# Kernel tuning notes

Measured on AMD Instinct MI355X. Metric: run time of the kernel, lower is better.

## Reference

```python
import math
import jax, jax.numpy as jnp
from jax import lax
import numpy as np

THETA = 10.0      # spiking threshold
TAU_SR = 10.0     # SRM (psp) alpha-kernel time constant
TAU_REF = 1.0     # refractory alpha-kernel time constant
SCALE_REF = 2.0   # refractory scale (kernel = -scaleRef*theta*alpha)
TAU_RHO = 1.0     # surrogate-gradient width
TS = 1.0          # simulation time step


def _alpha_filter_scan(x, tau, extra_input_fn=None):
    """Causal convolution along last (time) axis with alpha kernel
    k[n] = (n*Ts/tau) * exp(1 - n*Ts/tau)  (k[0] = 0),
    implemented exactly as a 2-state linear recurrence.
    x: [N, C, T] -> out: [N, C, T]."""
    d = jnp.float32(math.exp(-TS / tau))
    c = jnp.float32(math.e * TS / tau)
    xT = jnp.moveaxis(x, -1, 0)  # [T, N, C]

    def step(carry, xt):
        p, a = carry
        a = d * (a + p)          # alpha response from inputs up to t-1
        p = d * p + xt           # pure exponential state
        return (p, a), a * c

    z = jnp.zeros_like(xT[0])
    _, out = lax.scan(step, (z, z), xT)
    return jnp.moveaxis(out, 0, -1)


def psp(x):
    return _alpha_filter_scan(x, TAU_SR)


@jax.custom_vjp
def spike_fn(v):
    # Heaviside threshold on (membrane - theta)
    return (v >= 0).astype(v.dtype)

def _spike_fwd(v):
    return spike_fn(v), v

def _spike_bwd(v, g):
    # SLAYER surrogate gradient: exponential pdf around threshold
    grad = (1.0 / TAU_RHO) * jnp.exp(-jnp.abs(v) / TAU_RHO)
    return (g * grad,)

spike_fn.defvjp(_spike_fwd, _spike_bwd)


def spike_layer(u_in):
    """Threshold-and-refract over time. u_in: [N, C, T] psp potentials.
    Refractory response = -scaleRef*theta * alpha_{tauRef}(past spikes)."""
    d = jnp.float32(math.exp(-TS / TAU_REF))
    c = jnp.float32(math.e * TS / TAU_REF)
    ref_scale = jnp.float32(-SCALE_REF * THETA)
    uT = jnp.moveaxis(u_in, -1, 0)  # [T, N, C]

    def step(carry, ut):
        p, a = carry
        a = d * (a + p)                      # refractory potential at t
        u = ut + c * a                       # membrane potential
        s = spike_fn(u - THETA)              # spikes (0/1)
        p = d * p + ref_scale * s            # inject refractory impulse
        return (p, a), s

    z = jnp.zeros_like(uT[0])
    _, s = lax.scan(step, (z, z), uT)
    return jnp.moveaxis(s, 0, -1)


def setup_inputs() -> dict:
    key = jax.random.key(0)
    k1, k2, k3 = jax.random.split(key, 3)
    N, I, H, O, T = 64, 256, 1024, 18, 500
    # Bernoulli(0.1) input spikes
    spike_input = (jax.random.uniform(k1, (N, I, T)) < 0.1).astype(jnp.float32)
    W1 = jax.random.normal(k2, (H, I), dtype=jnp.float32) * (1.0 / math.sqrt(I))
    W2 = jax.random.normal(k3, (O, H), dtype=jnp.float32) * (1.0 / math.sqrt(H))
    return {"spike_input": spike_input, "W1": W1, "W2": W2}


def reference(spike_input, W1, W2):
    # layer 1: dense (per-timestep linear) -> psp -> spike
    y1 = jnp.einsum('nit,hi->nht', spike_input, W1)
    s1 = spike_layer(psp(y1))
    # layer 2
    y2 = jnp.einsum('nht,oh->not', s1, W2)
    s2 = spike_layer(psp(y2))
    return s2
```

## Files before the change

kernel.cpp:

```cpp
#include <hip/hip_runtime.h>


#define NN 64
#define II 256
#define HH 1024
#define OO 18
#define TT 500

#define D_SR 0.9048374180359595f
#define C_SR 0.27182818284590454f
#define D_RF 0.36787944117144233f
#define C_RF 2.718281828459045f
#define THETA 10.0f
#define REFS (-20.0f)

typedef _Float16 f16;
typedef _Float16 f16x2 __attribute__((ext_vector_type(2)));
typedef _Float16 f16x8 __attribute__((ext_vector_type(8)));
typedef float f32x4 __attribute__((ext_vector_type(4)));

__device__ __forceinline__ void gl2lds16(const void* g, void* l) {
    __builtin_amdgcn_global_load_lds(
        (const __attribute__((address_space(1))) void*)g,
        (__attribute__((address_space(3))) void*)l, 16, 0, 0);
}

__launch_bounds__(256)
__global__ void prep_x(const float* __restrict__ X, f16* __restrict__ Xb) {
    __shared__ float tile[64][65];
    const int n = blockIdx.z, i0 = blockIdx.y * 64, t0 = blockIdx.x * 64;
    const int tx = threadIdx.x & 63, q = threadIdx.x >> 6;
    const float* Xn = X + (size_t)n * II * TT;
#pragma unroll 4
    for (int j = 0; j < 16; ++j) {
        int il = j * 4 + q;
        int t = t0 + tx;
        tile[il][tx] = (t < TT) ? Xn[(size_t)(i0 + il) * TT + t] : 0.f;
    }
    __syncthreads();
#pragma unroll 4
    for (int j = 0; j < 16; ++j) {
        int tl = j * 4 + q;
        int t = t0 + tl;
        if (t < TT)
            Xb[((size_t)n * TT + t) * II + i0 + tx] = (f16)tile[tx][tl];
    }
}

__launch_bounds__(256)
__global__ void prep_w1(const float* __restrict__ W1, f16* __restrict__ Wh,
                        f16* __restrict__ Wl) {
    int idx = blockIdx.x * 256 + threadIdx.x;
    float w = W1[idx];
    f16 h = (f16)w;
    f16 l = (f16)(w - (float)h);
    Wh[idx] = h;
    Wl[idx] = l;
}

__launch_bounds__(256)
__global__ void prep_w2(const float* __restrict__ W2, f16* __restrict__ Wh,
                        f16* __restrict__ Wl) {
    int idx = blockIdx.x * 256 + threadIdx.x;
    int o = idx >> 10;
    float w = (o < OO) ? W2[idx] : 0.f;
    f16 h = (f16)w;
    f16 l = (f16)(w - (float)h);
    Wh[idx] = h;
    Wl[idx] = l;
}

__launch_bounds__(256)
__global__ void gemm1_scan1(const f16* __restrict__ Xb, const f16* __restrict__ Wh,
                            const f16* __restrict__ Wl, f16* __restrict__ S1) {
    __shared__ __align__(16) char smem[128 * 132 * 4];
    float* yb = (float*)smem;

    const int tid = threadIdx.x;
    const int wave = tid >> 6, lane = tid & 63;

    const int f = blockIdx.y * 8 + blockIdx.x;
    const int x = f & 7, g = f >> 3;
    const int n = x * 8 + (g & 7);
    const int ht = g >> 3;
    const int h0g = ht * 128;

    const int rbl = wave * 32 + (lane >> 2);
    const int koff = (lane & 3) * 8;
    const f16* gBh0 = Wh + (size_t)(h0g + rbl) * II + koff;
    const f16* gBl0 = Wl + (size_t)(h0g + rbl) * II + koff;

    const int wm = wave & 1, wn = wave >> 1;
    const int fr = lane & 15, kq = lane >> 4;

    float p1 = 0.f, a1 = 0.f, p2 = 0.f, a2 = 0.f;

    for (int c = 0; c < 4; ++c) {
        const int t0 = c * 128;
        const int TCe = (TT - t0 < 128) ? (TT - t0) : 128;

        int r0 = rbl;      if (r0 > TCe - 1) r0 = TCe - 1;
        int r1 = rbl + 16; if (r1 > TCe - 1) r1 = TCe - 1;
        const f16* gA0 = Xb + ((size_t)n * TT + t0 + r0) * II + koff;
        const f16* gA1 = Xb + ((size_t)n * TT + t0 + r1) * II + koff;

        auto stage = [&](int kk2, int b) {
            f16* As_b = (f16*)(smem + b * 24576);
            f16* Bh_b = As_b + 4096;
            f16* Bl_b = As_b + 8192;
            const int ko = kk2 * 32;
            gl2lds16(gA0 + ko, As_b + wave * 1024);
            gl2lds16(gA1 + ko, As_b + wave * 1024 + 512);
            gl2lds16(gBh0 + ko, Bh_b + wave * 1024);
            gl2lds16(gBh0 + 16 * II + ko, Bh_b + wave * 1024 + 512);
            gl2lds16(gBl0 + ko, Bl_b + wave * 1024);
            gl2lds16(gBl0 + 16 * II + ko, Bl_b + wave * 1024 + 512);
        };

        stage(0, 0);

        f32x4 acc[4][4] = {};
        for (int kk = 0; kk < 8; ++kk) {
            __syncthreads();
            if (kk < 7) stage(kk + 1, (kk + 1) & 1);

            const f16* As_b = (const f16*)(smem + (kk & 1) * 24576);
            const f16* Bh_b = As_b + 4096;
            const f16* Bl_b = As_b + 8192;

            f16x8 av[4], bhv[4], blv[4];
#pragma unroll
            for (int i = 0; i < 4; ++i) {
                av[i]  = *(const f16x8*)(As_b + (wm * 64 + i * 16 + fr) * 32 + kq * 8);
                bhv[i] = *(const f16x8*)(Bh_b + (wn * 64 + i * 16 + fr) * 32 + kq * 8);
                blv[i] = *(const f16x8*)(Bl_b + (wn * 64 + i * 16 + fr) * 32 + kq * 8);
            }
#pragma unroll
            for (int i = 0; i < 4; ++i)
#pragma unroll
                for (int j = 0; j < 4; ++j) {
                    acc[i][j] = __builtin_amdgcn_mfma_f32_16x16x32_f16(av[i], bhv[j], acc[i][j], 0, 0, 0);
                    acc[i][j] = __builtin_amdgcn_mfma_f32_16x16x32_f16(av[i], blv[j], acc[i][j], 0, 0, 0);
                }
        }
        __syncthreads();

#pragma unroll
        for (int i = 0; i < 4; ++i)
#pragma unroll
            for (int j = 0; j < 4; ++j) {
                int tr = wm * 64 + i * 16 + kq * 4;
                int hc = wn * 64 + j * 16 + fr;
#pragma unroll
                for (int r = 0; r < 4; ++r)
                    yb[(tr + r) * 132 + hc] = acc[i][j][r];
            }
        __syncthreads();

        if (tid < 128) {
            f16* sq = S1 + ((size_t)n * TT + t0) * HH + h0g + tid;
            float rb_[8];
#pragma unroll
            for (int j = 0; j < 8; ++j) rb_[j] = yb[j * 132 + tid];
            int t = 0;
            for (; t + 8 <= TCe; t += 8) {
#pragma unroll
                for (int j = 0; j < 8; ++j) {
                    float xv = rb_[j];
                    int tn = t + j + 8;
                    rb_[j] = (tn < TCe) ? yb[tn * 132 + tid] : 0.f;
                    a1 = D_SR * (a1 + p1);
                    p1 = D_SR * p1 + xv;
                    float ut = C_SR * a1;
                    a2 = D_RF * (a2 + p2);
                    float u = ut + C_RF * a2;
                    float s = (u >= THETA) ? 1.0f : 0.0f;
                    p2 = D_RF * p2 + REFS * s;
                    sq[(size_t)(t + j) * HH] = (f16)s;
                }
            }
            int rem = TCe - t;
#pragma unroll
            for (int j = 0; j < 8; ++j) {
                if (j < rem) {
                    float xv = rb_[j];
                    a1 = D_SR * (a1 + p1);
                    p1 = D_SR * p1 + xv;
                    float ut = C_SR * a1;
                    a2 = D_RF * (a2 + p2);
                    float u = ut + C_RF * a2;
                    float s = (u >= THETA) ? 1.0f : 0.0f;
                    p2 = D_RF * p2 + REFS * s;
                    sq[(size_t)(t + j) * HH] = (f16)s;
                }
            }
        }
        __syncthreads();
    }
}

__launch_bounds__(256)
__global__ void gemm2_mfma(const f16* __restrict__ S1, const f16* __restrict__ W2h,
                           const f16* __restrict__ W2l, float* __restrict__ Y2) {
    __shared__ __align__(16) f16 As[2][64 * 32];
    __shared__ __align__(16) f16 Bh[2][32 * 32];
    __shared__ __align__(16) f16 Bl[2][32 * 32];

    const int tid = threadIdx.x;
    const int wave = tid >> 6, lane = tid & 63;
    const int m0 = blockIdx.x * 64;
    const int fr = lane & 15, kq = lane >> 4;

    const f16* gA = S1 + (size_t)(m0 + wave * 16 + (lane >> 2)) * HH + (lane & 3) * 8;
    const f16* gB = (wave < 2 ? W2h : W2l) + (size_t)((wave & 1) * 16 + (lane >> 2)) * HH + (lane & 3) * 8;

    auto stage = [&](int kk2, int b) {
        const int ko = kk2 * 32;
        gl2lds16(gA + ko, &As[b][wave * 512]);
        gl2lds16(gB + ko, (wave < 2 ? &Bh[b][0] : &Bl[b][0]) + (wave & 1) * 512);
    };

    stage(0, 0);

    f32x4 acc[2] = {};
    for (int kk = 0; kk < HH / 32; ++kk) {
        __syncthreads();
        if (kk < HH / 32 - 1) stage(kk + 1, (kk + 1) & 1);
        const int b = kk & 1;

        f16x8 a, bh[2], bl[2];
        a = *(const f16x8*)(&As[b][(wave * 16 + fr) * 32 + kq * 8]);
#pragma unroll
        for (int j = 0; j < 2; ++j) {
            bh[j] = *(const f16x8*)(&Bh[b][(j * 16 + fr) * 32 + kq * 8]);
            bl[j] = *(const f16x8*)(&Bl[b][(j * 16 + fr) * 32 + kq * 8]);
        }
#pragma unroll
        for (int j = 0; j < 2; ++j) {
            acc[j] = __builtin_amdgcn_mfma_f32_16x16x32_f16(a, bh[j], acc[j], 0, 0, 0);
            acc[j] = __builtin_amdgcn_mfma_f32_16x16x32_f16(a, bl[j], acc[j], 0, 0, 0);
        }
    }

#pragma unroll
    for (int j = 0; j < 2; ++j) {
        int rbase = m0 + wave * 16 + kq * 4;
        int cc = j * 16 + fr;
        float* p = Y2 + (size_t)rbase * 32 + cc;
#pragma unroll
        for (int r = 0; r < 4; ++r)
            p[(size_t)r * 32] = acc[j][r];
    }
}

__launch_bounds__(256)
__global__ void scan2_k(const float* __restrict__ Y2, float* __restrict__ Out) {
    __shared__ float yc[TT * 32];
    __shared__ float sb[OO * TT];
    const int n = blockIdx.x, tid = threadIdx.x;

    const float4* src = (const float4*)(Y2 + (size_t)n * TT * 32);
    float4* dst = (float4*)yc;
    for (int i = tid; i < TT * 8; i += 256) dst[i] = src[i];
    __syncthreads();

    if (tid < 32) {
        float p1 = 0.f, a1 = 0.f, p2 = 0.f, a2 = 0.f;
        float rb_[8];
#pragma unroll
        for (int j = 0; j < 8; ++j) rb_[j] = yc[j * 32 + tid];
        int t = 0;
        for (; t + 8 <= TT; t += 8) {
#pragma unroll
            for (int j = 0; j < 8; ++j) {
                float xv = rb_[j];
                int tn = t + j + 8;
                rb_[j] = (tn < TT) ? yc[tn * 32 + tid] : 0.f;
                a1 = D_SR * (a1 + p1);
                p1 = D_SR * p1 + xv;
                float ut = C_SR * a1;
                a2 = D_RF * (a2 + p2);
                float u = ut + C_RF * a2;
                float s = (u >= THETA) ? 1.0f : 0.0f;
                p2 = D_RF * p2 + REFS * s;
                if (tid < OO) sb[tid * TT + t + j] = s;
            }
        }
#pragma unroll
        for (int j = 0; j < 8; ++j) {
            if (t + j < TT) {
                float xv = rb_[j];
                a1 = D_SR * (a1 + p1);
                p1 = D_SR * p1 + xv;
                float ut = C_SR * a1;
                a2 = D_RF * (a2 + p2);
                float u = ut + C_RF * a2;
                float s = (u >= THETA) ? 1.0f : 0.0f;
                p2 = D_RF * p2 + REFS * s;
                if (tid < OO) sb[tid * TT + t + j] = s;
            }
        }
    }
    __syncthreads();

    float* on = Out + (size_t)n * OO * TT;
    for (int e = tid; e < OO * TT; e += 256) on[e] = sb[e];
}

extern "C" void kernel_launch(void* const* d_in, const int* in_sizes, int n_in,
                              void* d_out, int out_size, void* d_ws, size_t ws_size,
                              hipStream_t stream) {
    const float* X  = (const float*)d_in[0];
    const float* W1 = (const float*)d_in[1];
    const float* W2 = (const float*)d_in[2];
    float* out = (float*)d_out;

    const size_t s_s1 = (size_t)NN * TT * HH * 2;
    const size_t s_Xb = (size_t)NN * TT * II * 2;
    const size_t s_W  = (size_t)HH * II * 2;
    const size_t s_W2 = (size_t)32 * HH * 2;

    char* w = (char*)d_ws;
    f16*   s1b = (f16*)w;  w += s_s1;
    f16*   Xb  = (f16*)w;  w += s_Xb;
    f16*   W1h = (f16*)w;  w += s_W;
    f16*   W1l = (f16*)w;  w += s_W;
    f16*   W2h = (f16*)w;  w += s_W2;
    f16*   W2l = (f16*)w;  w += s_W2;
    float* y2  = (float*)w;

    prep_x<<<dim3(8, 4, NN), 256, 0, stream>>>(X, Xb);
    prep_w1<<<(HH * II) / 256, 256, 0, stream>>>(W1, W1h, W1l);
    prep_w2<<<(32 * HH) / 256, 256, 0, stream>>>(W2, W2h, W2l);

    gemm1_scan1<<<dim3(8, NN), 256, 0, stream>>>(Xb, W1h, W1l, s1b);

    gemm2_mfma<<<(NN * TT) / 64, 256, 0, stream>>>(s1b, W2h, W2l, y2);
    scan2_k<<<NN, 256, 0, stream>>>(y2, out);
}
```

Baseline: 196.6 us.

## Fuse second GEMM into gemm1_scan1 epilogue with per-tile partial sums

The layer-1 spike tensor is no longer written to global memory as f16 and then re-read by a separate gemm2 kernel. Each gemm1_scan1 block keeps its spikes in LDS and multiplies them by its 128-column slice of W2, pre-swizzled into the MFMA fragment layout. It writes an fp32 partial Y2 per H-tile, and scan2_k sums the 8 partials while loading. This removes a large global round trip and one launch, at the cost of extra MFMA and LDS work in the fused kernel plus an 8x larger partial buffer to reduce.

```diff
diff --git a/kernel.cpp b/kernel.cpp
--- a/kernel.cpp
+++ b/kernel.cpp
@@ -15,7 +15,6 @@
 #define REFS (-20.0f)
 
 typedef _Float16 f16;
-typedef _Float16 f16x2 __attribute__((ext_vector_type(2)));
 typedef _Float16 f16x8 __attribute__((ext_vector_type(8)));
 typedef float f32x4 __attribute__((ext_vector_type(4)));
 
@@ -59,20 +58,30 @@
 }
 
 __launch_bounds__(256)
-__global__ void prep_w2(const float* __restrict__ W2, f16* __restrict__ Wh,
-                        f16* __restrict__ Wl) {
+__global__ void prep_w2f(const float* __restrict__ W2, f16* __restrict__ Wfh,
+                         f16* __restrict__ Wfl) {
     int idx = blockIdx.x * 256 + threadIdx.x;
-    int o = idx >> 10;
-    float w = (o < OO) ? W2[idx] : 0.f;
-    f16 h = (f16)w;
-    f16 l = (f16)(w - (float)h);
-    Wh[idx] = h;
-    Wl[idx] = l;
+    int kq = idx & 3, fr = (idx >> 2) & 15, kk = (idx >> 6) & 3;
+    int j = (idx >> 8) & 1, ht = idx >> 9;
+    int o = j * 16 + fr;
+    int h0 = ht * 128 + kk * 32 + kq * 8;
+    f16x8 h, l;
+#pragma unroll
+    for (int e = 0; e < 8; ++e) {
+        float w = (o < OO) ? W2[(size_t)o * HH + h0 + e] : 0.f;
+        f16 hh = (f16)w;
+        h[e] = hh;
+        l[e] = (f16)(w - (float)hh);
+    }
+    size_t dst = ((size_t)ht * 8 + j * 4 + kk) * 512 + fr * 32 + kq * 8;
+    *(f16x8*)(Wfh + dst) = h;
+    *(f16x8*)(Wfl + dst) = l;
 }
 
 __launch_bounds__(256)
 __global__ void gemm1_scan1(const f16* __restrict__ Xb, const f16* __restrict__ Wh,
-                            const f16* __restrict__ Wl, f16* __restrict__ S1) {
+                            const f16* __restrict__ Wl, const f16* __restrict__ W2fh,
+                            const f16* __restrict__ W2fl, float* __restrict__ Y2p) {
     __shared__ __align__(16) char smem[128 * 132 * 4];
     float* yb = (float*)smem;
 
@@ -92,6 +101,9 @@
 
     const int wm = wave & 1, wn = wave >> 1;
     const int fr = lane & 15, kq = lane >> 4;
+
+    const f16* bfh = W2fh + (size_t)ht * 4096 + fr * 32 + kq * 8;
+    const f16* bfl = W2fl + (size_t)ht * 4096 + fr * 32 + kq * 8;
 
     float p1 = 0.f, a1 = 0.f, p2 = 0.f, a2 = 0.f;
 
@@ -158,7 +170,6 @@
         __syncthreads();
 
         if (tid < 128) {
-            f16* sq = S1 + ((size_t)n * TT + t0) * HH + h0g + tid;
             float rb_[8];
 #pragma unroll
             for (int j = 0; j < 8; ++j) rb_[j] = yb[j * 132 + tid];
@@ -176,7 +187,7 @@
                     float u = ut + C_RF * a2;
                     float s = (u >= THETA) ? 1.0f : 0.0f;
                     p2 = D_RF * p2 + REFS * s;
-                    sq[(size_t)(t + j) * HH] = (f16)s;
+                    yb[(t + j) * 132 + tid] = s;
                 }
             }
             int rem = TCe - t;
@@ -191,77 +202,76 @@
                     float u = ut + C_RF * a2;
                     float s = (u >= THETA) ? 1.0f : 0.0f;
                     p2 = D_RF * p2 + REFS * s;
-                    sq[(size_t)(t + j) * HH] = (f16)s;
+                    yb[(t + j) * 132 + tid] = s;
                 }
             }
         }
         __syncthreads();
-    }
-}
-
-__launch_bounds__(256)
-__global__ void gemm2_mfma(const f16* __restrict__ S1, const f16* __restrict__ W2h,
-                           const f16* __restrict__ W2l, float* __restrict__ Y2) {
-    __shared__ __align__(16) f16 As[2][64 * 32];
-    __shared__ __align__(16) f16 Bh[2][32 * 32];
-    __shared__ __align__(16) f16 Bl[2][32 * 32];
-
-    const int tid = threadIdx.x;
-    const int wave = tid >> 6, lane = tid & 63;
-    const int m0 = blockIdx.x * 64;
-    const int fr = lane & 15, kq = lane >> 4;
-
-    const f16* gA = S1 + (size_t)(m0 + wave * 16 + (lane >> 2)) * HH + (lane & 3) * 8;
-    const f16* gB = (wave < 2 ? W2h : W2l) + (size_t)((wave & 1) * 16 + (lane >> 2)) * HH + (lane & 3) * 8;
-
-    auto stage = [&](int kk2, int b) {
-        const int ko = kk2 * 32;
-        gl2lds16(gA + ko, &As[b][wave * 512]);
-        gl2lds16(gB + ko, (wave < 2 ? &Bh[b][0] : &Bl[b][0]) + (wave & 1) * 512);
-    };
-
-    stage(0, 0);
-
-    f32x4 acc[2] = {};
-    for (int kk = 0; kk < HH / 32; ++kk) {
+
+        {
+            f16x8 bh2[2][4], bl2[2][4];
+#pragma unroll
+            for (int j = 0; j < 2; ++j)
+#pragma unroll
+                for (int kk = 0; kk < 4; ++kk) {
+                    bh2[j][kk] = *(const f16x8*)(bfh + (j * 4 + kk) * 512);
+                    bl2[j][kk] = *(const f16x8*)(bfl + (j * 4 + kk) * 512);
+                }
+#pragma unroll
+            for (int i = 0; i < 2; ++i) {
+                f16x8 sf[4];
+#pragma unroll
+                for (int kk = 0; kk < 4; ++kk) {
+                    const float* sp = yb + (wave * 32 + i * 16 + fr) * 132 + kk * 32 + kq * 8;
+                    float4 v0 = *(const float4*)(sp);
+                    float4 v1 = *(const float4*)(sp + 4);
+                    f16x8 tv;
+                    tv[0] = (f16)v0.x; tv[1] = (f16)v0.y; tv[2] = (f16)v0.z; tv[3] = (f16)v0.w;
+                    tv[4] = (f16)v1.x; tv[5] = (f16)v1.y; tv[6] = (f16)v1.z; tv[7] = (f16)v1.w;
+                    sf[kk] = tv;
+                }
+                f32x4 acc2[2] = {};
+#pragma unroll
+                for (int kk = 0; kk < 4; ++kk)
+#pragma unroll
+                    for (int j = 0; j < 2; ++j) {
+                        acc2[j] = __builtin_amdgcn_mfma_f32_16x16x32_f16(sf[kk], bh2[j][kk], acc2[j], 0, 0, 0);
+                        acc2[j] = __builtin_amdgcn_mfma_f32_16x16x32_f16(sf[kk], bl2[j][kk], acc2[j], 0, 0, 0);
+                    }
+                const int rbase = wave * 32 + i * 16 + kq * 4;
+#pragma unroll
+                for (int j = 0; j < 2; ++j) {
+#pragma unroll
+                    for (int r = 0; r < 4; ++r) {
+                        int t = t0 + rbase + r;
+                        if (t < TT)
+                            Y2p[(((size_t)ht * NN + n) * TT + t) * 32 + j * 16 + fr] = acc2[j][r];
+                    }
+                }
+            }
+        }
         __syncthreads();
-        if (kk < HH / 32 - 1) stage(kk + 1, (kk + 1) & 1);
-        const int b = kk & 1;
-
-        f16x8 a, bh[2], bl[2];
-        a = *(const f16x8*)(&As[b][(wave * 16 + fr) * 32 + kq * 8]);
-#pragma unroll
-        for (int j = 0; j < 2; ++j) {
-            bh[j] = *(const f16x8*)(&Bh[b][(j * 16 + fr) * 32 + kq * 8]);
-            bl[j] = *(const f16x8*)(&Bl[b][(j * 16 + fr) * 32 + kq * 8]);
-        }
-#pragma unroll
-        for (int j = 0; j < 2; ++j) {
-            acc[j] = __builtin_amdgcn_mfma_f32_16x16x32_f16(a, bh[j], acc[j], 0, 0, 0);
-            acc[j] = __builtin_amdgcn_mfma_f32_16x16x32_f16(a, bl[j], acc[j], 0, 0, 0);
-        }
-    }
-
-#pragma unroll
-    for (int j = 0; j < 2; ++j) {
-        int rbase = m0 + wave * 16 + kq * 4;
-        int cc = j * 16 + fr;
-        float* p = Y2 + (size_t)rbase * 32 + cc;
-#pragma unroll
-        for (int r = 0; r < 4; ++r)
-            p[(size_t)r * 32] = acc[j][r];
-    }
-}
-
-__launch_bounds__(256)
-__global__ void scan2_k(const float* __restrict__ Y2, float* __restrict__ Out) {
+    }
+}
+
+__launch_bounds__(256)
+__global__ void scan2_k(const float* __restrict__ Y2p, float* __restrict__ Out) {
     __shared__ float yc[TT * 32];
     __shared__ float sb[OO * TT];
     const int n = blockIdx.x, tid = threadIdx.x;
 
-    const float4* src = (const float4*)(Y2 + (size_t)n * TT * 32);
+    const float4* s0 = (const float4*)(Y2p + (size_t)n * TT * 32);
+    const size_t hstr = (size_t)NN * TT * 32 / 4;
     float4* dst = (float4*)yc;
-    for (int i = tid; i < TT * 8; i += 256) dst[i] = src[i];
+    for (int i = tid; i < TT * 8; i += 256) {
+        float4 a = s0[i];
+#pragma unroll
+        for (int ht = 1; ht < 8; ++ht) {
+            float4 b = s0[i + (size_t)ht * hstr];
+            a.x += b.x; a.y += b.y; a.z += b.z; a.w += b.w;
+        }
+        dst[i] = a;
+    }
     __syncthreads();
 
     if (tid < 32) {
@@ -315,26 +325,24 @@
     const float* W2 = (const float*)d_in[2];
     float* out = (float*)d_out;
 
-    const size_t s_s1 = (size_t)NN * TT * HH * 2;
-    const size_t s_Xb = (size_t)NN * TT * II * 2;
-    const size_t s_W  = (size_t)HH * II * 2;
-    const size_t s_W2 = (size_t)32 * HH * 2;
+    const size_t s_y2p = (size_t)8 * NN * TT * 32 * 4;
+    const size_t s_Xb  = (size_t)NN * TT * II * 2;
+    const size_t s_W   = (size_t)HH * II * 2;
+    const size_t s_W2f = (size_t)8 * 4096 * 2;
 
     char* w = (char*)d_ws;
-    f16*   s1b = (f16*)w;  w += s_s1;
-    f16*   Xb  = (f16*)w;  w += s_Xb;
-    f16*   W1h = (f16*)w;  w += s_W;
-    f16*   W1l = (f16*)w;  w += s_W;
-    f16*   W2h = (f16*)w;  w += s_W2;
-    f16*   W2l = (f16*)w;  w += s_W2;
-    float* y2  = (float*)w;
+    float* y2p  = (float*)w;  w += s_y2p;
+    f16*   Xb   = (f16*)w;    w += s_Xb;
+    f16*   W1h  = (f16*)w;    w += s_W;
+    f16*   W1l  = (f16*)w;    w += s_W;
+    f16*   W2fh = (f16*)w;    w += s_W2f;
+    f16*   W2fl = (f16*)w;    w += s_W2f;
 
     prep_x<<<dim3(8, 4, NN), 256, 0, stream>>>(X, Xb);
     prep_w1<<<(HH * II) / 256, 256, 0, stream>>>(W1, W1h, W1l);
-    prep_w2<<<(32 * HH) / 256, 256, 0, stream>>>(W2, W2h, W2l);
-
-    gemm1_scan1<<<dim3(8, NN), 256, 0, stream>>>(Xb, W1h, W1l, s1b);
-
-    gemm2_mfma<<<(NN * TT) / 64, 256, 0, stream>>>(s1b, W2h, W2l, y2);
-    scan2_k<<<NN, 256, 0, stream>>>(y2, out);
-}
+    prep_w2f<<<16, 256, 0, stream>>>(W2, W2fh, W2fl);
+
+    gemm1_scan1<<<dim3(8, NN), 256, 0, stream>>>(Xb, W1h, W1l, W2fh, W2fl, y2p);
+
+    scan2_k<<<NN, 256, 0, stream>>>(y2p, out);
+}
```

After: 226.4 us. +15.1%, slower.
